# Kernel tuning notes

Hardware: AMD Instinct MI355X
Metric: run time of the kernel (lower is better)

The kernel has to match this reference:

```python
import jax, jax.numpy as jnp
import numpy as np

MOMENTUM = 0.05
EPS = 1e-06


def _gated_ema(x, g):
    """y[t] = (1 - g[t]) * y[t-1] + g[t] * x[t], y[-1] = 0.
    x: (B, C, T), g: (B, 1, T) -> (B, C, T)"""
    xT = jnp.moveaxis(x, -1, 0)  # (T, B, C)
    gT = jnp.moveaxis(g, -1, 0)  # (T, B, 1)
    init = jnp.zeros(x.shape[:-1], x.dtype)  # (B, C)

    def step(carry, inp):
        xt, gt = inp
        carry = (1.0 - gt) * carry + gt * xt
        return carry, carry

    _, ys = jax.lax.scan(step, init, (xT, gT))
    return jnp.moveaxis(ys, 0, -1)


def setup_inputs() -> dict:
    key = jax.random.key(0)
    ks = jax.random.split(key, 6)
    B, C, T = 8, 512, 8192
    return {
        "x": jax.random.normal(ks[0], (B, C, T), dtype=jnp.float32),
        "g": jax.random.uniform(ks[1], (B, 1, T), dtype=jnp.float32),
        "Wa_w": jax.random.normal(ks[2], (1, C, 1), dtype=jnp.float32),
        "Wb_w": jax.random.normal(ks[3], (1, C, 1), dtype=jnp.float32),
        "Wo_w": jax.random.normal(ks[4], (C, 1, 1), dtype=jnp.float32),
        "Wo_b": jax.random.normal(ks[5], (C,), dtype=jnp.float32),
    }


def reference(x, g, Wa_w, Wb_w, Wo_w, Wo_b):
    sg = jax.lax.stop_gradient
    C = x.shape[1]
    g = g * MOMENTUM  # time-varying momentum gate
    # Wa: 1x1 conv C->1 with softmax over input channels (convex combination)
    wa = jax.nn.softmax(Wa_w, axis=1)  # (1, C, 1)
    mean = jnp.sum(wa * _gated_ema(sg(x), g), axis=1, keepdims=True)  # (B, 1, T)
    xc = x - mean
    wb = jax.nn.softmax(Wb_w, axis=1)  # (1, C, 1)
    var = jnp.sum(wb * _gated_ema(jnp.square(sg(xc)), g), axis=1, keepdims=True)  # (B, 1, T)
    xn = xc / jnp.sqrt(var + EPS)
    # Wo: grouped 1x1 conv (groups=C) == per-channel scale + bias
    return xn * Wo_w.reshape(1, C, 1) + Wo_b.reshape(1, C, 1)
```

## Files before the change

kernel.cpp:

```cpp
#include <hip/hip_runtime.h>

constexpr int BB = 8, CC = 512, TT = 8192;
static_assert((TT & (TT - 1)) == 0 && (CC & (CC - 1)) == 0, "pow2");
constexpr int LOG_T = 13, LOG_C = 9;
constexpr float MOM = 0.05f, EPSV = 1e-6f;

typedef float v4f __attribute__((ext_vector_type(4)));

__global__ __launch_bounds__(512) void k_reduce_c(const float* __restrict__ x,
                                                  const float* __restrict__ Wa,
                                                  const float* __restrict__ Wb,
                                                  float* __restrict__ sa,
                                                  float* __restrict__ sb,
                                                  float* __restrict__ sb2) {
  __shared__ float lwa[CC];
  __shared__ float lwb[CC];
  __shared__ float xw[32];
  __shared__ float red[3][8][256];
  const int tid = threadIdx.x;
  const int lane = tid & 63;
  const int wid = tid >> 6;

  float va = Wa[tid], vb = Wb[tid];
  float ma = va, mb = vb;
  #pragma unroll
  for (int off = 32; off > 0; off >>= 1) {
    ma = fmaxf(ma, __shfl_down(ma, off, 64));
    mb = fmaxf(mb, __shfl_down(mb, off, 64));
  }
  if (lane == 0) { xw[wid] = ma; xw[8 + wid] = mb; }
  __syncthreads();
  ma = xw[0]; mb = xw[8];
  #pragma unroll
  for (int w = 1; w < 8; ++w) { ma = fmaxf(ma, xw[w]); mb = fmaxf(mb, xw[8 + w]); }
  float ea = expf(va - ma), eb = expf(vb - mb);
  float sA = ea, sB = eb;
  #pragma unroll
  for (int off = 32; off > 0; off >>= 1) {
    sA += __shfl_down(sA, off, 64);
    sB += __shfl_down(sB, off, 64);
  }
  if (lane == 0) { xw[16 + wid] = sA; xw[24 + wid] = sB; }
  __syncthreads();
  sA = xw[16]; sB = xw[24];
  #pragma unroll
  for (int w = 1; w < 8; ++w) { sA += xw[16 + w]; sB += xw[24 + w]; }
  lwa[tid] = ea * (1.f / sA);
  lwb[tid] = eb * (1.f / sB);
  __syncthreads();

  const int tilesPerB = TT / 256;
  const int b = blockIdx.x / tilesPerB;
  const int tbase = (blockIdx.x % tilesPerB) * 256;
  const int t = tbase + lane * 4;
  const int cbase = wid * 64;
  const float* xp = x + ((size_t)(b * CC + cbase)) * TT + t;

  float a0=0,a1=0,a2=0,a3=0;
  float b0=0,b1=0,b2=0,b3=0;
  float q0=0,q1=0,q2=0,q3=0;
  #pragma unroll 8
  for (int cc = 0; cc < 64; ++cc) {
    float4 xv = *(const float4*)(xp + (size_t)cc * TT);
    float wac = lwa[cbase + cc];
    float wbc = lwb[cbase + cc];
    a0 = fmaf(wac, xv.x, a0); a1 = fmaf(wac, xv.y, a1);
    a2 = fmaf(wac, xv.z, a2); a3 = fmaf(wac, xv.w, a3);
    b0 = fmaf(wbc, xv.x, b0); b1 = fmaf(wbc, xv.y, b1);
    b2 = fmaf(wbc, xv.z, b2); b3 = fmaf(wbc, xv.w, b3);
    q0 = fmaf(wbc * xv.x, xv.x, q0); q1 = fmaf(wbc * xv.y, xv.y, q1);
    q2 = fmaf(wbc * xv.z, xv.z, q2); q3 = fmaf(wbc * xv.w, xv.w, q3);
  }
  const int li = lane * 4;
  red[0][wid][li+0]=a0; red[0][wid][li+1]=a1; red[0][wid][li+2]=a2; red[0][wid][li+3]=a3;
  red[1][wid][li+0]=b0; red[1][wid][li+1]=b1; red[1][wid][li+2]=b2; red[1][wid][li+3]=b3;
  red[2][wid][li+0]=q0; red[2][wid][li+1]=q1; red[2][wid][li+2]=q2; red[2][wid][li+3]=q3;
  __syncthreads();

  if (tid < 64) {
    const int o = tid * 4;
    float oa[4] = {0,0,0,0}, ob[4] = {0,0,0,0}, oq[4] = {0,0,0,0};
    #pragma unroll
    for (int w = 0; w < 8; ++w) {
      #pragma unroll
      for (int k = 0; k < 4; ++k) {
        oa[k] += red[0][w][o+k];
        ob[k] += red[1][w][o+k];
        oq[k] += red[2][w][o+k];
      }
    }
    const size_t dst = (size_t)b * TT + tbase + o;
    *(float4*)(sa  + dst) = make_float4(oa[0], oa[1], oa[2], oa[3]);
    *(float4*)(sb  + dst) = make_float4(ob[0], ob[1], ob[2], ob[3]);
    *(float4*)(sb2 + dst) = make_float4(oq[0], oq[1], oq[2], oq[3]);
  }
}

__device__ __forceinline__ float affine_scan_prev(float A, float B, int tid,
                                                  float* wAs, float* wBs) {
  const int lane = tid & 63;
  const int wid = tid >> 6;
  #pragma unroll
  for (int off = 1; off < 64; off <<= 1) {
    float pA = __shfl_up(A, off, 64);
    float pB = __shfl_up(B, off, 64);
    if (lane >= off) { B = fmaf(A, pB, B); A *= pA; }
  }
  __syncthreads();
  if (lane == 63) { wAs[wid] = A; wBs[wid] = B; }
  __syncthreads();
  float cB = 0.f;
  for (int w = 0; w < wid; ++w) cB = fmaf(wAs[w], cB, wBs[w]);
  float leA = __shfl_up(A, 1, 64);
  float leB = __shfl_up(B, 1, 64);
  if (lane == 0) { leA = 1.f; leB = 0.f; }
  return fmaf(leA, cB, leB);
}

__global__ __launch_bounds__(1024) void k_scan(const float* __restrict__ g,
                                               const float* __restrict__ sa,
                                               const float* __restrict__ sb,
                                               const float* __restrict__ sb2,
                                               float* __restrict__ mean,
                                               float* __restrict__ inv) {
  constexpr int CH = 8;
  __shared__ float wAs[16], wBs[16];
  const int tid = threadIdx.x;
  const size_t base = (size_t)blockIdx.x * TT + (size_t)tid * CH;

  float gv[CH], av[CH], bv[CH], qv[CH];
  *(float4*)(gv)     = *(const float4*)(g   + base);
  *(float4*)(gv + 4) = *(const float4*)(g   + base + 4);
  *(float4*)(av)     = *(const float4*)(sa  + base);
  *(float4*)(av + 4) = *(const float4*)(sa  + base + 4);
  *(float4*)(bv)     = *(const float4*)(sb  + base);
  *(float4*)(bv + 4) = *(const float4*)(sb  + base + 4);
  *(float4*)(qv)     = *(const float4*)(sb2 + base);
  *(float4*)(qv + 4) = *(const float4*)(sb2 + base + 4);

  float gt[CH], pa[CH];
  float A = 1.f, Bv = 0.f;
  #pragma unroll
  for (int j = 0; j < CH; ++j) {
    float gg = gv[j] * MOM;
    gt[j] = gg;
    float p = gg * av[j];
    pa[j] = p;
    float a = 1.f - gg;
    A *= a;
    Bv = fmaf(a, Bv, p);
  }
  float m = affine_scan_prev(A, Bv, tid, wAs, wBs);

  float m4[CH];
  float A2 = 1.f, B2 = 0.f;
  #pragma unroll
  for (int j = 0; j < CH; ++j) {
    float a = 1.f - gt[j];
    m = fmaf(a, m, pa[j]);
    m4[j] = m;
    float vi = fmaf(m, m, fmaf(-2.f * m, bv[j], qv[j]));
    float pv = gt[j] * vi;
    pa[j] = pv;
    A2 *= a;
    B2 = fmaf(a, B2, pv);
  }
  *(float4*)(mean + base)     = *(float4*)(m4);
  *(float4*)(mean + base + 4) = *(float4*)(m4 + 4);

  float v = affine_scan_prev(A2, B2, tid, wAs, wBs);

  float i4[CH];
  #pragma unroll
  for (int j = 0; j < CH; ++j) {
    v = fmaf(1.f - gt[j], v, pa[j]);
    i4[j] = rsqrtf(v + EPSV);
  }
  *(float4*)(inv + base)     = *(float4*)(i4);
  *(float4*)(inv + base + 4) = *(float4*)(i4 + 4);
}

__global__ __launch_bounds__(256) void k_out(const float* __restrict__ x,
                                             const float* __restrict__ mean,
                                             const float* __restrict__ inv,
                                             const float* __restrict__ wo,
                                             const float* __restrict__ bo,
                                             float* __restrict__ out) {
  const size_t base4 = (size_t)blockIdx.x * 1024 + threadIdx.x;
  #pragma unroll
  for (int j = 0; j < 4; ++j) {
    const size_t idx = base4 + (size_t)j * 256;
    const size_t flat = idx * 4;
    const int t = (int)(flat & (TT - 1));
    const size_t rem = flat >> LOG_T;
    const int c = (int)(rem & (CC - 1));
    const int b = (int)(rem >> LOG_C);
    float4 xv = *(const float4*)(x + flat);
    const size_t mi = ((size_t)b << LOG_T) + t;
    float4 m4 = *(const float4*)(mean + mi);
    float4 i4 = *(const float4*)(inv + mi);
    const float w = wo[c], bb = bo[c];
    v4f o;
    o.x = fmaf((xv.x - m4.x) * i4.x, w, bb);
    o.y = fmaf((xv.y - m4.y) * i4.y, w, bb);
    o.z = fmaf((xv.z - m4.z) * i4.z, w, bb);
    o.w = fmaf((xv.w - m4.w) * i4.w, w, bb);
    __builtin_nontemporal_store(o, (v4f*)(out + flat));
  }
}

extern "C" void kernel_launch(void* const* d_in, const int* in_sizes, int n_in,
                              void* d_out, int out_size, void* d_ws, size_t ws_size,
                              hipStream_t stream) {
  const float* x    = (const float*)d_in[0];
  const float* g    = (const float*)d_in[1];
  const float* Wa_w = (const float*)d_in[2];
  const float* Wb_w = (const float*)d_in[3];
  const float* Wo_w = (const float*)d_in[4];
  const float* Wo_b = (const float*)d_in[5];
  float* out = (float*)d_out;

  constexpr int BT = BB * TT;
  float* ws   = (float*)d_ws;
  float* sa   = ws;
  float* sb   = sa + BT;
  float* sb2  = sb + BT;
  float* mean = sb2 + BT;
  float* inv  = mean + BT;

  k_reduce_c<<<BB * (TT / 256), 512, 0, stream>>>(x, Wa_w, Wb_w, sa, sb, sb2);
  k_scan<<<BB, 1024, 0, stream>>>(g, sa, sb, sb2, mean, inv);
  k_out<<<8192, 256, 0, stream>>>(x, mean, inv, Wo_w, Wo_b, out);
}
```

Baseline: 82.52 us.

## Fuse reduce, scan and output into one kernel with decoupled lookback

The three kernels (channel reduction, time scan, normalization) become one kernel with 1024 blocks, each handling a 64-step time tile. Each block keeps its x tile in registers, publishes its affine scan aggregate with a flag, and resolves its prefix by spinning on the flags of all earlier tiles. This removes the second read of x, the round trips of the intermediate arrays, and two launches. In exchange it relies on earlier blocks being scheduled first to avoid deadlock, adds a memset per call, and serialises the lookback over up to 127 predecessors.

```diff
diff --git a/kernel.cpp b/kernel.cpp
--- a/kernel.cpp
+++ b/kernel.cpp
@@ -1,234 +1,202 @@
 #include <hip/hip_runtime.h>
 
 constexpr int BB = 8, CC = 512, TT = 8192;
-static_assert((TT & (TT - 1)) == 0 && (CC & (CC - 1)) == 0, "pow2");
-constexpr int LOG_T = 13, LOG_C = 9;
+constexpr int TILE = 64;
+constexpr int TPB = TT / TILE;
+constexpr int NBLK = BB * TPB;
 constexpr float MOM = 0.05f, EPSV = 1e-6f;
 
 typedef float v4f __attribute__((ext_vector_type(4)));
 
-__global__ __launch_bounds__(512) void k_reduce_c(const float* __restrict__ x,
-                                                  const float* __restrict__ Wa,
-                                                  const float* __restrict__ Wb,
-                                                  float* __restrict__ sa,
-                                                  float* __restrict__ sb,
-                                                  float* __restrict__ sb2) {
-  __shared__ float lwa[CC];
-  __shared__ float lwb[CC];
-  __shared__ float xw[32];
-  __shared__ float red[3][8][256];
-  const int tid = threadIdx.x;
-  const int lane = tid & 63;
-  const int wid = tid >> 6;
-
-  float va = Wa[tid], vb = Wb[tid];
-  float ma = va, mb = vb;
-  #pragma unroll
-  for (int off = 32; off > 0; off >>= 1) {
-    ma = fmaxf(ma, __shfl_down(ma, off, 64));
-    mb = fmaxf(mb, __shfl_down(mb, off, 64));
-  }
-  if (lane == 0) { xw[wid] = ma; xw[8 + wid] = mb; }
-  __syncthreads();
-  ma = xw[0]; mb = xw[8];
-  #pragma unroll
-  for (int w = 1; w < 8; ++w) { ma = fmaxf(ma, xw[w]); mb = fmaxf(mb, xw[8 + w]); }
-  float ea = expf(va - ma), eb = expf(vb - mb);
-  float sA = ea, sB = eb;
-  #pragma unroll
-  for (int off = 32; off > 0; off >>= 1) {
-    sA += __shfl_down(sA, off, 64);
-    sB += __shfl_down(sB, off, 64);
-  }
-  if (lane == 0) { xw[16 + wid] = sA; xw[24 + wid] = sB; }
-  __syncthreads();
-  sA = xw[16]; sB = xw[24];
-  #pragma unroll
-  for (int w = 1; w < 8; ++w) { sA += xw[16 + w]; sB += xw[24 + w]; }
-  lwa[tid] = ea * (1.f / sA);
-  lwb[tid] = eb * (1.f / sB);
-  __syncthreads();
-
-  const int tilesPerB = TT / 256;
-  const int b = blockIdx.x / tilesPerB;
-  const int tbase = (blockIdx.x % tilesPerB) * 256;
-  const int t = tbase + lane * 4;
-  const int cbase = wid * 64;
-  const float* xp = x + ((size_t)(b * CC + cbase)) * TT + t;
-
-  float a0=0,a1=0,a2=0,a3=0;
-  float b0=0,b1=0,b2=0,b3=0;
-  float q0=0,q1=0,q2=0,q3=0;
-  #pragma unroll 8
-  for (int cc = 0; cc < 64; ++cc) {
-    float4 xv = *(const float4*)(xp + (size_t)cc * TT);
-    float wac = lwa[cbase + cc];
-    float wbc = lwb[cbase + cc];
-    a0 = fmaf(wac, xv.x, a0); a1 = fmaf(wac, xv.y, a1);
-    a2 = fmaf(wac, xv.z, a2); a3 = fmaf(wac, xv.w, a3);
-    b0 = fmaf(wbc, xv.x, b0); b1 = fmaf(wbc, xv.y, b1);
-    b2 = fmaf(wbc, xv.z, b2); b3 = fmaf(wbc, xv.w, b3);
-    q0 = fmaf(wbc * xv.x, xv.x, q0); q1 = fmaf(wbc * xv.y, xv.y, q1);
-    q2 = fmaf(wbc * xv.z, xv.z, q2); q3 = fmaf(wbc * xv.w, xv.w, q3);
-  }
-  const int li = lane * 4;
-  red[0][wid][li+0]=a0; red[0][wid][li+1]=a1; red[0][wid][li+2]=a2; red[0][wid][li+3]=a3;
-  red[1][wid][li+0]=b0; red[1][wid][li+1]=b1; red[1][wid][li+2]=b2; red[1][wid][li+3]=b3;
-  red[2][wid][li+0]=q0; red[2][wid][li+1]=q1; red[2][wid][li+2]=q2; red[2][wid][li+3]=q3;
-  __syncthreads();
-
-  if (tid < 64) {
-    const int o = tid * 4;
-    float oa[4] = {0,0,0,0}, ob[4] = {0,0,0,0}, oq[4] = {0,0,0,0};
-    #pragma unroll
-    for (int w = 0; w < 8; ++w) {
-      #pragma unroll
-      for (int k = 0; k < 4; ++k) {
-        oa[k] += red[0][w][o+k];
-        ob[k] += red[1][w][o+k];
-        oq[k] += red[2][w][o+k];
-      }
-    }
-    const size_t dst = (size_t)b * TT + tbase + o;
-    *(float4*)(sa  + dst) = make_float4(oa[0], oa[1], oa[2], oa[3]);
-    *(float4*)(sb  + dst) = make_float4(ob[0], ob[1], ob[2], ob[3]);
-    *(float4*)(sb2 + dst) = make_float4(oq[0], oq[1], oq[2], oq[3]);
-  }
-}
-
-__device__ __forceinline__ float affine_scan_prev(float A, float B, int tid,
-                                                  float* wAs, float* wBs) {
-  const int lane = tid & 63;
-  const int wid = tid >> 6;
+__device__ __forceinline__ void wave_incl_affine(float& A, float& B) {
+  const int lane = threadIdx.x & 63;
   #pragma unroll
   for (int off = 1; off < 64; off <<= 1) {
     float pA = __shfl_up(A, off, 64);
     float pB = __shfl_up(B, off, 64);
     if (lane >= off) { B = fmaf(A, pB, B); A *= pA; }
   }
+}
+
+__device__ __forceinline__ float lookback(const float* __restrict__ wsA,
+                                          const float* __restrict__ wsB,
+                                          const int* __restrict__ fl,
+                                          int rec0, int tile) {
+  const int lane = threadIdx.x & 63;
+  const int j0 = 2 * lane, j1 = j0 + 1;
+  float A = 1.f, B = 0.f;
+  if (j0 < tile) {
+    while (__hip_atomic_load(&fl[rec0 + j0], __ATOMIC_ACQUIRE,
+                             __HIP_MEMORY_SCOPE_AGENT) == 0)
+      __builtin_amdgcn_s_sleep(2);
+    A = __hip_atomic_load(&wsA[rec0 + j0], __ATOMIC_RELAXED, __HIP_MEMORY_SCOPE_AGENT);
+    B = __hip_atomic_load(&wsB[rec0 + j0], __ATOMIC_RELAXED, __HIP_MEMORY_SCOPE_AGENT);
+  }
+  if (j1 < tile) {
+    while (__hip_atomic_load(&fl[rec0 + j1], __ATOMIC_ACQUIRE,
+                             __HIP_MEMORY_SCOPE_AGENT) == 0)
+      __builtin_amdgcn_s_sleep(2);
+    const float A1v = __hip_atomic_load(&wsA[rec0 + j1], __ATOMIC_RELAXED, __HIP_MEMORY_SCOPE_AGENT);
+    const float B1v = __hip_atomic_load(&wsB[rec0 + j1], __ATOMIC_RELAXED, __HIP_MEMORY_SCOPE_AGENT);
+    B = fmaf(A1v, B, B1v);
+    A *= A1v;
+  }
+  wave_incl_affine(A, B);
+  return __shfl(B, 63, 64);
+}
+
+__global__ __launch_bounds__(512) void k_fused(
+    const float* __restrict__ x, const float* __restrict__ g,
+    const float* __restrict__ Wa, const float* __restrict__ Wb,
+    const float* __restrict__ Wo, const float* __restrict__ Bo,
+    float* __restrict__ out,
+    float* __restrict__ A1, float* __restrict__ B1,
+    float* __restrict__ A2, float* __restrict__ B2,
+    int* __restrict__ f1, int* __restrict__ f2) {
+  __shared__ float lwa[CC], lwb[CC], lwo[CC], lbo[CC];
+  __shared__ float red[3][8][TILE];
+  __shared__ float xw[32];
+  __shared__ float mean_s[TILE], inv_s[TILE];
+
+  const int tid = threadIdx.x;
+  const int lane = tid & 63;
+  const int wid = tid >> 6;
+  const int bidx = blockIdx.x;
+  const int b = bidx >> 7;
+  const int tile = bidx & (TPB - 1);
+  const int rec0 = b << 7;
+  const int t0 = tile * TILE;
+
+  const int t4 = (lane & 15) << 2;
+  const int csub = lane >> 4;
+  const int c0 = (wid << 6) + csub;
+  const float* xrow = x + (size_t)b * CC * TT + t0 + t4;
+  v4f xv[16];
+  #pragma unroll
+  for (int i = 0; i < 16; ++i)
+    xv[i] = *(const v4f*)(xrow + (size_t)(c0 + (i << 2)) * TT);
+
+  {
+    float va = Wa[tid], vb = Wb[tid];
+    lwo[tid] = Wo[tid];
+    lbo[tid] = Bo[tid];
+    float ma = va, mb = vb;
+    #pragma unroll
+    for (int off = 32; off > 0; off >>= 1) {
+      ma = fmaxf(ma, __shfl_down(ma, off, 64));
+      mb = fmaxf(mb, __shfl_down(mb, off, 64));
+    }
+    if (lane == 0) { xw[wid] = ma; xw[8 + wid] = mb; }
+    __syncthreads();
+    ma = xw[0]; mb = xw[8];
+    #pragma unroll
+    for (int w = 1; w < 8; ++w) { ma = fmaxf(ma, xw[w]); mb = fmaxf(mb, xw[8 + w]); }
+    const float ea = expf(va - ma), eb = expf(vb - mb);
+    float sA = ea, sB = eb;
+    #pragma unroll
+    for (int off = 32; off > 0; off >>= 1) {
+      sA += __shfl_down(sA, off, 64);
+      sB += __shfl_down(sB, off, 64);
+    }
+    if (lane == 0) { xw[16 + wid] = sA; xw[24 + wid] = sB; }
+    __syncthreads();
+    sA = xw[16]; sB = xw[24];
+    #pragma unroll
+    for (int w = 1; w < 8; ++w) { sA += xw[16 + w]; sB += xw[24 + w]; }
+    lwa[tid] = ea * (1.f / sA);
+    lwb[tid] = eb * (1.f / sB);
+  }
   __syncthreads();
-  if (lane == 63) { wAs[wid] = A; wBs[wid] = B; }
+
+  v4f aa = {0.f, 0.f, 0.f, 0.f}, ab = aa, aq = aa;
+  #pragma unroll
+  for (int i = 0; i < 16; ++i) {
+    const int c = c0 + (i << 2);
+    const float wac = lwa[c], wbc = lwb[c];
+    aa += wac * xv[i];
+    ab += wbc * xv[i];
+    aq += (wbc * xv[i]) * xv[i];
+  }
+  #pragma unroll
+  for (int k = 0; k < 4; ++k) {
+    aa[k] += __shfl_xor(aa[k], 16, 64);
+    ab[k] += __shfl_xor(ab[k], 16, 64);
+    aq[k] += __shfl_xor(aq[k], 16, 64);
+    aa[k] += __shfl_xor(aa[k], 32, 64);
+    ab[k] += __shfl_xor(ab[k], 32, 64);
+    aq[k] += __shfl_xor(aq[k], 32, 64);
+  }
+  if (lane < 16) {
+    *(v4f*)&red[0][wid][t4] = aa;
+    *(v4f*)&red[1][wid][t4] = ab;
+    *(v4f*)&red[2][wid][t4] = aq;
+  }
   __syncthreads();
-  float cB = 0.f;
-  for (int w = 0; w < wid; ++w) cB = fmaf(wAs[w], cB, wBs[w]);
-  float leA = __shfl_up(A, 1, 64);
-  float leB = __shfl_up(B, 1, 64);
-  if (lane == 0) { leA = 1.f; leB = 0.f; }
-  return fmaf(leA, cB, leB);
-}
-
-__global__ __launch_bounds__(1024) void k_scan(const float* __restrict__ g,
-                                               const float* __restrict__ sa,
-                                               const float* __restrict__ sb,
-                                               const float* __restrict__ sb2,
-                                               float* __restrict__ mean,
-                                               float* __restrict__ inv) {
-  constexpr int CH = 8;
-  __shared__ float wAs[16], wBs[16];
-  const int tid = threadIdx.x;
-  const size_t base = (size_t)blockIdx.x * TT + (size_t)tid * CH;
-
-  float gv[CH], av[CH], bv[CH], qv[CH];
-  *(float4*)(gv)     = *(const float4*)(g   + base);
-  *(float4*)(gv + 4) = *(const float4*)(g   + base + 4);
-  *(float4*)(av)     = *(const float4*)(sa  + base);
-  *(float4*)(av + 4) = *(const float4*)(sa  + base + 4);
-  *(float4*)(bv)     = *(const float4*)(sb  + base);
-  *(float4*)(bv + 4) = *(const float4*)(sb  + base + 4);
-  *(float4*)(qv)     = *(const float4*)(sb2 + base);
-  *(float4*)(qv + 4) = *(const float4*)(sb2 + base + 4);
-
-  float gt[CH], pa[CH];
-  float A = 1.f, Bv = 0.f;
-  #pragma unroll
-  for (int j = 0; j < CH; ++j) {
-    float gg = gv[j] * MOM;
-    gt[j] = gg;
-    float p = gg * av[j];
-    pa[j] = p;
-    float a = 1.f - gg;
-    A *= a;
-    Bv = fmaf(a, Bv, p);
-  }
-  float m = affine_scan_prev(A, Bv, tid, wAs, wBs);
-
-  float m4[CH];
-  float A2 = 1.f, B2 = 0.f;
-  #pragma unroll
-  for (int j = 0; j < CH; ++j) {
-    float a = 1.f - gt[j];
-    m = fmaf(a, m, pa[j]);
-    m4[j] = m;
-    float vi = fmaf(m, m, fmaf(-2.f * m, bv[j], qv[j]));
-    float pv = gt[j] * vi;
-    pa[j] = pv;
-    A2 *= a;
-    B2 = fmaf(a, B2, pv);
-  }
-  *(float4*)(mean + base)     = *(float4*)(m4);
-  *(float4*)(mean + base + 4) = *(float4*)(m4 + 4);
-
-  float v = affine_scan_prev(A2, B2, tid, wAs, wBs);
-
-  float i4[CH];
-  #pragma unroll
-  for (int j = 0; j < CH; ++j) {
-    v = fmaf(1.f - gt[j], v, pa[j]);
-    i4[j] = rsqrtf(v + EPSV);
-  }
-  *(float4*)(inv + base)     = *(float4*)(i4);
-  *(float4*)(inv + base + 4) = *(float4*)(i4 + 4);
-}
-
-__global__ __launch_bounds__(256) void k_out(const float* __restrict__ x,
-                                             const float* __restrict__ mean,
-                                             const float* __restrict__ inv,
-                                             const float* __restrict__ wo,
-                                             const float* __restrict__ bo,
-                                             float* __restrict__ out) {
-  const size_t base4 = (size_t)blockIdx.x * 1024 + threadIdx.x;
-  #pragma unroll
-  for (int j = 0; j < 4; ++j) {
-    const size_t idx = base4 + (size_t)j * 256;
-    const size_t flat = idx * 4;
-    const int t = (int)(flat & (TT - 1));
-    const size_t rem = flat >> LOG_T;
-    const int c = (int)(rem & (CC - 1));
-    const int b = (int)(rem >> LOG_C);
-    float4 xv = *(const float4*)(x + flat);
-    const size_t mi = ((size_t)b << LOG_T) + t;
-    float4 m4 = *(const float4*)(mean + mi);
-    float4 i4 = *(const float4*)(inv + mi);
-    const float w = wo[c], bb = bo[c];
-    v4f o;
-    o.x = fmaf((xv.x - m4.x) * i4.x, w, bb);
-    o.y = fmaf((xv.y - m4.y) * i4.y, w, bb);
-    o.z = fmaf((xv.z - m4.z) * i4.z, w, bb);
-    o.w = fmaf((xv.w - m4.w) * i4.w, w, bb);
-    __builtin_nontemporal_store(o, (v4f*)(out + flat));
+
+  if (wid == 0) {
+    const int t = lane;
+    float sa = 0.f, sbv = 0.f, sq = 0.f;
+    #pragma unroll
+    for (int w = 0; w < 8; ++w) {
+      sa  += red[0][w][t];
+      sbv += red[1][w][t];
+      sq  += red[2][w][t];
+    }
+    const float gt = g[(size_t)b * TT + t0 + t] * MOM;
+    const float a = 1.f - gt;
+
+    float Ai = a, Bi = gt * sa;
+    wave_incl_affine(Ai, Bi);
+    if (lane == 63) {
+      A1[bidx] = Ai; B1[bidx] = Bi;
+      __hip_atomic_store(&f1[bidx], 1, __ATOMIC_RELEASE, __HIP_MEMORY_SCOPE_AGENT);
+    }
+    const float mprev = (tile > 0) ? lookback(A1, B1, f1, rec0, tile) : 0.f;
+    const float m = fmaf(Ai, mprev, Bi);
+    mean_s[t] = m;
+
+    const float vi = fmaf(m, m, fmaf(-2.f * m, sbv, sq));
+    float Ci = a, Di = gt * vi;
+    wave_incl_affine(Ci, Di);
+    if (lane == 63) {
+      A2[bidx] = Ci; B2[bidx] = Di;
+      __hip_atomic_store(&f2[bidx], 1, __ATOMIC_RELEASE, __HIP_MEMORY_SCOPE_AGENT);
+    }
+    const float vprev = (tile > 0) ? lookback(A2, B2, f2, rec0, tile) : 0.f;
+    const float vv = fmaf(Ci, vprev, Di);
+    inv_s[t] = rsqrtf(vv + EPSV);
+  }
+  __syncthreads();
+
+  const v4f mval = *(const v4f*)&mean_s[t4];
+  const v4f ival = *(const v4f*)&inv_s[t4];
+  float* orow = out + (size_t)b * CC * TT + t0 + t4;
+  #pragma unroll
+  for (int i = 0; i < 16; ++i) {
+    const int c = c0 + (i << 2);
+    v4f o = (xv[i] - mval) * ival * lwo[c] + lbo[c];
+    *(v4f*)(orow + (size_t)c * TT) = o;
   }
 }
 
 extern "C" void kernel_launch(void* const* d_in, const int* in_sizes, int n_in,
                               void* d_out, int out_size, void* d_ws, size_t ws_size,
                               hipStream_t stream) {
-  const float* x    = (const float*)d_in[0];
-  const float* g    = (const float*)d_in[1];
-  const float* Wa_w = (const float*)d_in[2];
-  const float* Wb_w = (const float*)d_in[3];
-  const float* Wo_w = (const float*)d_in[4];
-  const float* Wo_b = (const float*)d_in[5];
+  const float* x  = (const float*)d_in[0];
+  const float* g  = (const float*)d_in[1];
+  const float* Wa = (const float*)d_in[2];
+  const float* Wb = (const float*)d_in[3];
+  const float* Wo = (const float*)d_in[4];
+  const float* Bo = (const float*)d_in[5];
   float* out = (float*)d_out;
 
-  constexpr int BT = BB * TT;
-  float* ws   = (float*)d_ws;
-  float* sa   = ws;
-  float* sb   = sa + BT;
-  float* sb2  = sb + BT;
-  float* mean = sb2 + BT;
-  float* inv  = mean + BT;
-
-  k_reduce_c<<<BB * (TT / 256), 512, 0, stream>>>(x, Wa_w, Wb_w, sa, sb, sb2);
-  k_scan<<<BB, 1024, 0, stream>>>(g, sa, sb, sb2, mean, inv);
-  k_out<<<8192, 256, 0, stream>>>(x, mean, inv, Wo_w, Wo_b, out);
-}
+  int* f1 = (int*)d_ws;
+  int* f2 = f1 + NBLK;
+  float* A1 = (float*)(f2 + NBLK);
+  float* B1 = A1 + NBLK;
+  float* A2 = B1 + NBLK;
+  float* B2 = A2 + NBLK;
+
+  hipMemsetAsync(d_ws, 0, 2 * NBLK * sizeof(int), stream);
+  k_fused<<<NBLK, 512, 0, stream>>>(x, g, Wa, Wb, Wo, Bo, out, A1, B1, A2, B2, f1, f2);
+}
```

New measurement: 153.7 us. 1.86x slower.
